# Kernel tuning notes

Hardware: AMD Instinct MI355X
Metric: run time of the kernel (lower is better)

The kernel has to match this reference:

```python
import jax, jax.numpy as jnp
import numpy as np

N = 120000
GRID = (480, 360, 32)
C_IN, C0, C1 = 16, 32, 64
EPS = 1e-5


def _build_rulebook(coords, lut, offsets, grid, n):
    # coords: [N,3] active voxel coords; lut: dense linear-index -> row (n = inactive)
    g = np.array(grid)
    cols = []
    for off in offsets:
        nc = coords + np.array(off)
        valid = np.all((nc >= 0) & (nc < g), axis=1)
        ncl = np.clip(nc, 0, g - 1)
        nlin = np.ravel_multi_index((ncl[:, 0], ncl[:, 1], ncl[:, 2]), grid)
        cols.append(np.where(valid, lut[nlin], n))
    return np.stack(cols, axis=1).astype(np.int32)  # [N, 9]


def setup_inputs() -> dict:
    rng = np.random.default_rng(0)
    total = GRID[0] * GRID[1] * GRID[2]
    lin = rng.choice(total, N, replace=False)
    coords = np.stack(np.unravel_index(lin, GRID), axis=1)
    lut = np.full(total, N, dtype=np.int32)
    lut[lin] = np.arange(N, dtype=np.int32)
    offs133 = [(0, dy, dz) for dy in (-1, 0, 1) for dz in (-1, 0, 1)]  # kernel (1,3,3)
    offs313 = [(dx, 0, dz) for dx in (-1, 0, 1) for dz in (-1, 0, 1)]  # kernel (3,1,3)
    nbr133 = jnp.asarray(_build_rulebook(coords, lut, offs133, GRID, N))
    nbr313 = jnp.asarray(_build_rulebook(coords, lut, offs313, GRID, N))

    key = jax.random.key(0)
    ks = jax.random.split(key, 9)

    def w(k, ci, co):
        return jax.random.normal(k, (9, ci, co), jnp.float32) * (1.0 / np.sqrt(9 * ci))

    ones = lambda c: jnp.ones((c,), jnp.float32)
    zeros = lambda c: jnp.zeros((c,), jnp.float32)
    return dict(
        x=jax.random.normal(ks[0], (N, C_IN), jnp.float32),
        nbr133=nbr133, nbr313=nbr313,
        W_c1=w(ks[1], C_IN, C0), g0=ones(C0), b0=zeros(C0),
        W_c12=w(ks[2], C0, C0), g02=ones(C0), b02=zeros(C0),
        W_c2=w(ks[3], C_IN, C0),
        W_c3=w(ks[4], C0, C0), g2=ones(C0), b2=zeros(C0),
        W_r1=w(ks[5], C0, C1), rg0=ones(C1), rb0=zeros(C1),
        W_r12=w(ks[6], C1, C1), rg02=ones(C1), rb02=zeros(C1),
        W_r2=w(ks[7], C0, C1), rg1=ones(C1), rb1=zeros(C1),
        W_r3=w(ks[8], C1, C1), rg2=ones(C1), rb2=zeros(C1),
    )


def _subm(x, nbr, W):
    # submanifold conv as rulebook gather-GEMM: pad row N with zeros for missing neighbors
    xp = jnp.concatenate([x, jnp.zeros((1, x.shape[1]), x.dtype)], axis=0)
    return jnp.einsum('nkc,kcd->nd', xp[nbr], W)  # [N, Cout]


def _bn(x, g, b):
    # BatchNorm1d over active voxels (training-mode batch stats, biased var)
    m = x.mean(axis=0)
    v = x.var(axis=0)
    return (x - m) / jnp.sqrt(v + EPS) * g + b


_lrelu = jax.nn.leaky_relu  # slope 0.01 = torch default


def reference(x, nbr133, nbr313, W_c1, g0, b0, W_c12, g02, b02, W_c2, W_c3, g2, b2,
              W_r1, rg0, rb0, W_r12, rg02, rb02, W_r2, rg1, rb1, W_r3, rg2, rb2):
    # ResContextBlock(16->32): conv -> act -> bn chains
    s = _bn(_lrelu(_subm(x, nbr133, W_c1)), g0, b0)
    s = _bn(_lrelu(_subm(s, nbr313, W_c12)), g02, b02)
    r = _lrelu(_subm(x, nbr313, W_c2))  # bn1 result discarded in source (reaA typo) -> faithfully skipped
    r = _bn(_lrelu(_subm(r, nbr133, W_c3)), g2, b2)
    y = r + s
    # ResBlock(32->64, pooling=False)
    s2 = _bn(_lrelu(_subm(y, nbr313, W_r1)), rg0, rb0)
    s2 = _bn(_lrelu(_subm(s2, nbr133, W_r12)), rg02, rb02)
    r2 = _bn(_lrelu(_subm(y, nbr133, W_r2)), rg1, rb1)
    r2 = _bn(_lrelu(_subm(r2, nbr313, W_r3)), rg2, rb2)
    return r2 + s2  # [N, 64]
```

## Files before the change

kernel.cpp:

```cpp
#include <hip/hip_runtime.h>
#include <hip/hip_bf16.h>

#define N_VOX 120000
#define NTILES (N_VOX / 16)

typedef __attribute__((ext_vector_type(8))) __bf16 bf16x8;
typedef __attribute__((ext_vector_type(4))) float floatx4;
using bf16 = __hip_bfloat16;

__device__ __forceinline__ float b2f(bf16 v) { return __bfloat162float(v); }
__device__ __forceinline__ bf16 f2b(float v) { return __float2bfloat16(v); }

__device__ __forceinline__ bf16x8 gload16(const bf16* p) {
    bf16x8 r;
    asm volatile("global_load_dwordx4 %0, %1, off" : "=v"(r) : "v"(p));
    return r;
}
__device__ __forceinline__ int gloadi(const int* p) {
    int r;
    asm volatile("global_load_dword %0, %1, off" : "=v"(r) : "v"(p));
    return r;
}
__device__ __forceinline__ void gstore16(bf16* p, bf16x8 v) {
    asm volatile("global_store_dwordx4 %0, %1, off" :: "v"(p), "v"(v) : "memory");
}
__device__ __forceinline__ void vm_wait0() { asm volatile("s_waitcnt vmcnt(0)" ::: "memory"); }
__device__ __forceinline__ void vm_wait1() { asm volatile("s_waitcnt vmcnt(1)" ::: "memory"); }
__device__ __forceinline__ void vm_wait2() { asm volatile("s_waitcnt vmcnt(2)" ::: "memory"); }
__device__ __forceinline__ void vm_wait3() { asm volatile("s_waitcnt vmcnt(3)" ::: "memory"); }
__device__ __forceinline__ void pin(bf16x8& x) { asm volatile("" : "+v"(x)); }
__device__ __forceinline__ void pini(int& x)   { asm volatile("" : "+v"(x)); }

template<int CIN, int COUT, int NW>
__device__ __forceinline__ void conv_body(
    const bf16* __restrict__ uin,
    const int*  __restrict__ nbr,
    const bf16* __restrict__ bpack,
    bf16* __restrict__ tout,
    float* __restrict__ stats, int bid, int nblk)
{
    constexpr int NT = COUT / 16;
    constexpr int K = 9 * CIN;
    constexpr int KSTEPS = (K + 31) / 32;
    constexpr bool BLDS = (COUT == 64);
    constexpr int NFRAG = KSTEPS * NT;
    constexpr int NSTORE = (16 * COUT) / 512;

    __shared__ bf16x8 Bs[BLDS ? NFRAG * 64 : 1];
    __shared__ int idxb[NW][2][192];
    __shared__ __align__(16) bf16 tbuf[NW][16 * COUT];
    __shared__ float sS[64], sS2[64];

    const int lane = threadIdx.x & 63;
    const int wave = threadIdx.x >> 6;
    const int m    = lane & 15;
    const int quad = lane >> 4;

    if (threadIdx.x < 64) { sS[threadIdx.x] = 0.f; sS2[threadIdx.x] = 0.f; }

    const bf16x8* bp = reinterpret_cast<const bf16x8*>(bpack);
    bf16x8 Bf[BLDS ? 1 : NFRAG];
    if constexpr (BLDS) {
        for (int f = threadIdx.x; f < NFRAG * 64; f += NW * 64) Bs[f] = bp[f];
    } else {
#pragma unroll
        for (int f = 0; f < NFRAG; ++f) Bf[f] = bp[f * 64 + lane];
    }
    __syncthreads();

    float ssum[NT], ssum2[NT];
#pragma unroll
    for (int c = 0; c < NT; ++c) { ssum[c] = 0.f; ssum2[c] = 0.f; }

    const int STRIDE = nblk * NW;
    const int t0 = bid * NW + wave;

    {
        const int* b0 = nbr + (size_t)t0 * 144;
        int i0 = gloadi(b0 + lane);
        int i1 = gloadi(b0 + 64 + lane);
        int i2 = gloadi(b0 + 128 + (lane & 15));
        vm_wait0();
        pini(i0); pini(i1); pini(i2);
        int* ib = idxb[wave][0];
        ib[lane] = i0; ib[64 + lane] = i1; ib[128 + (lane & 15)] = i2;
    }

    int p = 0;
    for (int tile = t0; tile < NTILES; tile += STRIDE) {
        const int* ib = idxb[wave][p];
        int idx[9];
#pragma unroll
        for (int nb = 0; nb < 9; ++nb) idx[nb] = ib[m * 9 + nb];

        bf16x8 a[KSTEPS];
#pragma unroll
        for (int t = 0; t < KSTEPS; ++t) {
            const bf16* src;
            if constexpr (CIN == 64) {
                src = uin + (((size_t)idx[t >> 1]) << 6) + ((t & 1) << 5) + quad * 8;
            } else if constexpr (CIN == 32) {
                src = uin + (((size_t)idx[t]) << 5) + quad * 8;
            } else {
                constexpr int KS = 9 * 16;
                const int j1 = (2 * t + 1 > 8) ? 8 : 2 * t + 1;
                int r_ = (quad & 2) ? idx[j1] : idx[2 * t];
                if (t * 32 + 24 >= KS) {
                    if (t * 32 + quad * 8 >= KS) r_ = N_VOX;
                }
                src = uin + (((size_t)r_) << 4) + ((quad & 1) << 3);
            }
            a[t] = gload16(src);
        }

        const int tnext = (tile + STRIDE < NTILES) ? tile + STRIDE : tile;
        const int* bn_ = nbr + (size_t)tnext * 144;
        int i0 = gloadi(bn_ + lane);
        int i1 = gloadi(bn_ + 64 + lane);
        int i2 = gloadi(bn_ + 128 + (lane & 15));

        vm_wait3();
#pragma unroll
        for (int t = 0; t < KSTEPS; ++t) pin(a[t]);

        floatx4 acc[NT];
#pragma unroll
        for (int c = 0; c < NT; ++c) acc[c] = (floatx4){0.f, 0.f, 0.f, 0.f};
#pragma unroll
        for (int t = 0; t < KSTEPS; ++t) {
#pragma unroll
            for (int c = 0; c < NT; ++c) {
                const bf16x8 b = BLDS ? Bs[(t * NT + c) * 64 + lane] : Bf[t * NT + c];
                acc[c] = __builtin_amdgcn_mfma_f32_16x16x32_bf16(a[t], b, acc[c], 0, 0, 0);
            }
        }

        bf16* tb = tbuf[wave];
#pragma unroll
        for (int c = 0; c < NT; ++c) {
            float ps = 0.f, ps2 = 0.f;
#pragma unroll
            for (int i = 0; i < 4; ++i) {
                float v = acc[c][i];
                v = v > 0.f ? v : 0.01f * v;
                tb[(quad * 4 + i) * COUT + c * 16 + m] = f2b(v);
                ps += v; ps2 += v * v;
            }
            ssum[c] += ps; ssum2[c] += ps2;
        }
#pragma unroll
        for (int g = 0; g < NSTORE; ++g) {
            const int off = g * 512 + lane * 8;
            bf16x8 row = *reinterpret_cast<const bf16x8*>(tb + off);
            gstore16(tout + (size_t)tile * (16 * COUT) + off, row);
        }

        if constexpr (NSTORE == 2) vm_wait2(); else vm_wait1();
        pini(i0); pini(i1); pini(i2);
        int* ibn = idxb[wave][p ^ 1];
        ibn[lane] = i0; ibn[64 + lane] = i1; ibn[128 + (lane & 15)] = i2;
        p ^= 1;
    }

    if (stats != nullptr) {
#pragma unroll
        for (int c = 0; c < NT; ++c) {
            atomicAdd(&sS[c * 16 + m], ssum[c]);
            atomicAdd(&sS2[c * 16 + m], ssum2[c]);
        }
        __syncthreads();
        if (threadIdx.x < COUT) {
            atomicAdd(&stats[threadIdx.x],      sS[threadIdx.x]);
            atomicAdd(&stats[64 + threadIdx.x], sS2[threadIdx.x]);
        }
    }
}

template<int CIN, int COUT, int NW>
__global__ __launch_bounds__(NW * 64) void conv_kernel(
    const bf16* __restrict__ uin, const int* __restrict__ nbr,
    const bf16* __restrict__ bpack, bf16* __restrict__ tout,
    float* __restrict__ stats)
{
    conv_body<CIN, COUT, NW>(uin, nbr, bpack, tout, stats, blockIdx.x, gridDim.x);
}

template<int CIN, int COUT, int NW>
__global__ __launch_bounds__(NW * 64) void conv2_kernel(
    int GA,
    const bf16* uinA, const int* nbrA, const bf16* bpA, bf16* toutA, float* stA,
    const bf16* uinB, const int* nbrB, const bf16* bpB, bf16* toutB, float* stB)
{
    const bool isB = (int)blockIdx.x >= GA;
    const int bid = isB ? (int)blockIdx.x - GA : (int)blockIdx.x;
    const bf16* uin   = isB ? uinB : uinA;
    const int*  nbr   = isB ? nbrB : nbrA;
    const bf16* bpack = isB ? bpB  : bpA;
    bf16*       tout  = isB ? toutB : toutA;
    float*      stats = isB ? stB  : stA;
    conv_body<CIN, COUT, NW>(uin, nbr, bpack, tout, stats, bid, GA);
}

template<int C>
__device__ __forceinline__ void bnapply_body(
    bf16* t, const float* __restrict__ s,
    const float* __restrict__ g, const float* __restrict__ b, int bid)
{
    __shared__ float pa[64], pc[64];
    if (threadIdx.x < C) {
        const float inv_n = 1.0f / N_VOX;
        const float mu = s[threadIdx.x] * inv_n;
        const float var = fmaxf(s[64 + threadIdx.x] * inv_n - mu * mu, 0.f);
        const float a = rsqrtf(var + 1e-5f) * g[threadIdx.x];
        pa[threadIdx.x] = a;
        pc[threadIdx.x] = b[threadIdx.x] - mu * a;
    }
    __syncthreads();
    const int i8 = (bid * 256 + threadIdx.x) * 8;
    if (i8 >= (N_VOX + 1) * C) return;
    if (i8 >= N_VOX * C) {
        uint4 z = {0, 0, 0, 0};
        *reinterpret_cast<uint4*>(t + i8) = z;
        return;
    }
    union { bf16x8 v; bf16 e[8]; } U, O;
    U.v = *reinterpret_cast<const bf16x8*>(t + i8);
    const int ch0 = i8 & (C - 1);
#pragma unroll
    for (int j = 0; j < 8; ++j)
        O.e[j] = f2b(pa[ch0 + j] * b2f(U.e[j]) + pc[ch0 + j]);
    *reinterpret_cast<bf16x8*>(t + i8) = O.v;
}

template<int C>
__global__ __launch_bounds__(256) void bnapply_kernel(
    bf16* t, const float* __restrict__ s,
    const float* __restrict__ g, const float* __restrict__ b)
{
    bnapply_body<C>(t, s, g, b, blockIdx.x);
}

__global__ __launch_bounds__(256) void bnapply2_kernel(
    int GA, bf16* tA, const float* sA, const float* gA, const float* bA,
    bf16* tB, const float* sB, const float* gB, const float* bB)
{
    const bool isB = (int)blockIdx.x >= GA;
    const int bid = isB ? (int)blockIdx.x - GA : (int)blockIdx.x;
    bnapply_body<64>(isB ? tB : tA, isB ? sB : sA, isB ? gB : gA,
                     isB ? bB : bA, bid);
}

template<int C, bool ZROW, typename OUT>
__global__ __launch_bounds__(256) void addbn_kernel(
    const bf16* ta, const float* __restrict__ sa,
    const float* __restrict__ ga, const float* __restrict__ ba,
    const bf16* tb, const float* __restrict__ sb,
    const float* __restrict__ gb, const float* __restrict__ bb,
    OUT* out)
{
    __shared__ float paa[64], pca[64], pab[64], pcb[64];
    if (threadIdx.x < C) {
        const float inv_n = 1.0f / N_VOX;
        const float ma = sa[threadIdx.x] * inv_n;
        const float va = fmaxf(sa[64 + threadIdx.x] * inv_n - ma * ma, 0.f);
        const float aa = rsqrtf(va + 1e-5f) * ga[threadIdx.x];
        paa[threadIdx.x] = aa;
        pca[threadIdx.x] = ba[threadIdx.x] - ma * aa;
        const float mb = sb[threadIdx.x] * inv_n;
        const float vb = fmaxf(sb[64 + threadIdx.x] * inv_n - mb * mb, 0.f);
        const float ab = rsqrtf(vb + 1e-5f) * gb[threadIdx.x];
        pab[threadIdx.x] = ab;
        pcb[threadIdx.x] = bb[threadIdx.x] - mb * ab;
    }
    __syncthreads();
    constexpr int TOTAL = (N_VOX + (ZROW ? 1 : 0)) * C;
    const int i8 = (blockIdx.x * 256 + threadIdx.x) * 8;
    if (i8 >= TOTAL) return;
    if (ZROW && i8 >= N_VOX * C) {
        uint4 z = {0, 0, 0, 0};
        *reinterpret_cast<uint4*>((bf16*)out + i8) = z;
        return;
    }
    union { bf16x8 v; bf16 e[8]; } A, B;
    A.v = *reinterpret_cast<const bf16x8*>(ta + i8);
    B.v = *reinterpret_cast<const bf16x8*>(tb + i8);
    const int ch0 = i8 & (C - 1);
    float r[8];
#pragma unroll
    for (int j = 0; j < 8; ++j)
        r[j] = paa[ch0 + j] * b2f(A.e[j]) + pca[ch0 + j]
             + pab[ch0 + j] * b2f(B.e[j]) + pcb[ch0 + j];
    if constexpr (sizeof(OUT) == 2) {
        union { bf16x8 v; bf16 e[8]; } O;
#pragma unroll
        for (int j = 0; j < 8; ++j) O.e[j] = f2b(r[j]);
        *reinterpret_cast<bf16x8*>(out + i8) = O.v;
    } else {
#pragma unroll
        for (int j = 0; j < 8; ++j) out[i8 + j] = r[j];
    }
}

#define PACK_TOTAL 139264
__global__ __launch_bounds__(256) void prep_kernel(
    const float* __restrict__ x,
    const float* W0, const float* W1, const float* W2, const float* W3,
    const float* W4, const float* W5, const float* W6, const float* W7,
    bf16* __restrict__ u0, bf16* __restrict__ bpack,
    float* __restrict__ stats, bf16* __restrict__ u3, bf16* __restrict__ u3b)
{
    const int gid = blockIdx.x * 256 + threadIdx.x;
    constexpr int NXE = (N_VOX + 1) * 16;
    if (gid < NXE) {
        u0[gid] = (gid < N_VOX * 16) ? f2b(x[gid]) : f2b(0.f);
        return;
    }
    int p = gid - NXE;
    if (p < PACK_TOTAL) {
        constexpr int cin[8]  = {16, 32, 16, 32, 32, 64, 32, 64};
        constexpr int cout[8] = {32, 32, 32, 32, 64, 64, 64, 64};
        constexpr int offs[9] = {0, 5120, 14336, 19456, 28672, 47104, 83968, 102400, 139264};
        const float* Ws[8] = {W0, W1, W2, W3, W4, W5, W6, W7};
        int w = 0;
        while (p >= offs[w + 1]) ++w;
        const int e = p - offs[w];
        const int CI = cin[w], CO = cout[w];
        const int NTl = CO / 16;
        const int j = e & 7;
        const int lane = (e >> 3) & 63;
        const int rest = e >> 9;
        const int c = rest % NTl;
        const int t = rest / NTl;
        const int ncol = c * 16 + (lane & 15);
        const int k = t * 32 + (lane >> 4) * 8 + j;
        float val = 0.f;
        if (k < 9 * CI) {
            const int nbq = k / CI;
            const int ci = k % CI;
            val = Ws[w][(nbq * CI + ci) * CO + ncol];
        }
        bpack[p] = f2b(val);
        return;
    }
    p -= PACK_TOTAL;
    if (p < 1024) { stats[p] = 0.f; return; }
    p -= 1024;
    if (p < 32) { u3[N_VOX * 32 + p] = f2b(0.f); return; }
    p -= 32;
    if (p < 32) u3b[N_VOX * 32 + p] = f2b(0.f);
}

extern "C" void kernel_launch(void* const* d_in, const int* in_sizes, int n_in,
                              void* d_out, int out_size, void* d_ws, size_t ws_size,
                              hipStream_t stream) {
    const float* x     = (const float*)d_in[0];
    const int* nbr133  = (const int*)d_in[1];
    const int* nbr313  = (const int*)d_in[2];
    const float* W_c1  = (const float*)d_in[3];
    const float* g0    = (const float*)d_in[4];
    const float* b0    = (const float*)d_in[5];
    const float* W_c12 = (const float*)d_in[6];
    const float* g02   = (const float*)d_in[7];
    const float* b02   = (const float*)d_in[8];
    const float* W_c2  = (const float*)d_in[9];
    const float* W_c3  = (const float*)d_in[10];
    const float* g2    = (const float*)d_in[11];
    const float* b2    = (const float*)d_in[12];
    const float* W_r1  = (const float*)d_in[13];
    const float* rg0   = (const float*)d_in[14];
    const float* rb0   = (const float*)d_in[15];
    const float* W_r12 = (const float*)d_in[16];
    const float* rg02  = (const float*)d_in[17];
    const float* rb02  = (const float*)d_in[18];
    const float* W_r2  = (const float*)d_in[19];
    const float* rg1   = (const float*)d_in[20];
    const float* rb1   = (const float*)d_in[21];
    const float* W_r3  = (const float*)d_in[22];
    const float* rg2   = (const float*)d_in[23];
    const float* rb2   = (const float*)d_in[24];

    char* ws = (char*)d_ws;
    size_t off = 0;
    auto alloc = [&](size_t bytes) -> char* {
        off = (off + 255) & ~(size_t)255;
        char* p = ws + off;
        off += bytes;
        return p;
    };
    const size_t NV = N_VOX;
    bf16* u0   = (bf16*)alloc((NV + 1) * 16 * 2);
    bf16* B1u3 = (bf16*)alloc((NV + 1) * 32 * 2);
    bf16* T4   = (bf16*)alloc(NV * 32 * 2);
    bf16* T2uy = (bf16*)alloc((NV + 1) * 32 * 2);
    bf16* B5B7 = (bf16*)alloc((NV + 1) * 64 * 2);
    bf16* T8   = (bf16*)alloc(NV * 64 * 2);
    bf16* bpack = (bf16*)alloc((size_t)PACK_TOTAL * 2);
    float* stats = (float*)alloc(1024 * 4);
    bf16* T9   = (bf16*)alloc(NV * 64 * 2);
    bf16* T6 = (bf16*)ws;

    float* st1 = stats + 0 * 128;
    float* st2 = stats + 1 * 128;
    float* st4 = stats + 3 * 128;
    float* st5 = stats + 4 * 128;
    float* st6 = stats + 5 * 128;
    float* st7 = stats + 6 * 128;
    float* st8 = stats + 7 * 128;

    bf16* bp0 = bpack + 0;
    bf16* bp1 = bpack + 5120;
    bf16* bp2 = bpack + 14336;
    bf16* bp3 = bpack + 19456;
    bf16* bp4 = bpack + 28672;
    bf16* bp5 = bpack + 47104;
    bf16* bp6 = bpack + 83968;
    bf16* bp7 = bpack + 102400;

    const int prep_total = (N_VOX + 1) * 16 + PACK_TOTAL + 1024 + 32 + 32;
    prep_kernel<<<(prep_total + 255) / 256, 256, 0, stream>>>(
        x, W_c1, W_c12, W_c2, W_c3, W_r1, W_r12, W_r2, W_r3,
        u0, bpack, stats, B1u3, T2uy);

    const int E32 = (((N_VOX + 1) * 32) / 8 + 255) / 256;
    const int E64 = (((N_VOX + 1) * 64) / 8 + 255) / 256;

    conv2_kernel<16, 32, 4><<<1536, 256, 0, stream>>>(
        768, u0, nbr133, bp0, B1u3, st1, u0, nbr313, bp2, T2uy, nullptr);
    bnapply_kernel<32><<<E32, 256, 0, stream>>>(B1u3, st1, g0, b0);
    conv2_kernel<32, 32, 4><<<1536, 256, 0, stream>>>(
        768, B1u3, nbr313, bp1, T4, st2, T2uy, nbr133, bp3, B5B7, st4);
    addbn_kernel<32, true, bf16><<<E32, 256, 0, stream>>>(
        T4, st2, g02, b02, B5B7, st4, g2, b2, T2uy);
    conv2_kernel<32, 64, 8><<<512, 512, 0, stream>>>(
        256, T2uy, nbr313, bp4, B5B7, st5, T2uy, nbr133, bp6, T8, st7);
    bnapply2_kernel<<<2 * E64, 256, 0, stream>>>(
        E64, B5B7, st5, rg0, rb0, T8, st7, rg1, rb1);
    conv2_kernel<64, 64, 16><<<256, 1024, 0, stream>>>(
        128, B5B7, nbr133, bp5, T6, st6, T8, nbr313, bp7, T9, st8);
    addbn_kernel<64, false, float><<<((N_VOX * 64 / 8) + 255) / 256, 256, 0, stream>>>(
        T6, st6, rg02, rb02, T9, st8, rg2, rb2, (float*)d_out);
}
```

Measured before the change: 261.3 us.

## Fold BatchNorm affine into next conv weights and per-neighbor bias

Removes the standalone BN-apply passes over the 32- and 64-channel activations. The BN scale is folded into repacked conv weights by small repack kernels, and the BN shift is applied as a per-neighbor bias added inside the conv only for valid neighbors. This saves full read-modify-write passes over large activation tensors. In exchange it adds small repack launches, bias-mask work in the conv epilogue, and extra LDS, and rounding now happens on the scaled weights rather than the normalized activations.

```diff
diff --git a/kernel.cpp b/kernel.cpp
--- a/kernel.cpp
+++ b/kernel.cpp
@@ -31,13 +31,15 @@
 __device__ __forceinline__ void pin(bf16x8& x) { asm volatile("" : "+v"(x)); }
 __device__ __forceinline__ void pini(int& x)   { asm volatile("" : "+v"(x)); }
 
-template<int CIN, int COUT, int NW>
+template<int CIN, int COUT, int NW, bool BIAS>
 __device__ __forceinline__ void conv_body(
     const bf16* __restrict__ uin,
     const int*  __restrict__ nbr,
     const bf16* __restrict__ bpack,
     bf16* __restrict__ tout,
-    float* __restrict__ stats, int bid, int nblk)
+    float* __restrict__ stats,
+    const float* __restrict__ biasT,
+    int bid, int nblk)
 {
     constexpr int NT = COUT / 16;
     constexpr int K = 9 * CIN;
@@ -50,6 +52,7 @@
     __shared__ int idxb[NW][2][192];
     __shared__ __align__(16) bf16 tbuf[NW][16 * COUT];
     __shared__ float sS[64], sS2[64];
+    __shared__ float biasL[BIAS ? 9 * COUT : 1];
 
     const int lane = threadIdx.x & 63;
     const int wave = threadIdx.x >> 6;
@@ -57,6 +60,12 @@
     const int quad = lane >> 4;
 
     if (threadIdx.x < 64) { sS[threadIdx.x] = 0.f; sS2[threadIdx.x] = 0.f; }
+
+    const bool useBias = BIAS && (biasT != nullptr);
+    if constexpr (BIAS) {
+        if (biasT != nullptr)
+            for (int f = threadIdx.x; f < 9 * COUT; f += NW * 64) biasL[f] = biasT[f];
+    }
 
     const bf16x8* bp = reinterpret_cast<const bf16x8*>(bpack);
     bf16x8 Bf[BLDS ? 1 : NFRAG];
@@ -135,6 +144,29 @@
             }
         }
 
+        if (useBias) {
+            unsigned vm_[4];
+#pragma unroll
+            for (int i = 0; i < 4; ++i) {
+                const int r = quad * 4 + i;
+                unsigned v = 0;
+#pragma unroll
+                for (int nb = 0; nb < 9; ++nb)
+                    v |= (ib[r * 9 + nb] != N_VOX) ? (1u << nb) : 0u;
+                vm_[i] = v;
+            }
+#pragma unroll
+            for (int c = 0; c < NT; ++c) {
+#pragma unroll
+                for (int nb = 0; nb < 9; ++nb) {
+                    const float bl = biasL[nb * COUT + c * 16 + m];
+#pragma unroll
+                    for (int i = 0; i < 4; ++i)
+                        acc[c][i] += ((vm_[i] >> nb) & 1u) ? bl : 0.f;
+                }
+            }
+        }
+
         bf16* tb = tbuf[wave];
 #pragma unroll
         for (int c = 0; c < NT; ++c) {
@@ -176,20 +208,13 @@
     }
 }
 
-template<int CIN, int COUT, int NW>
-__global__ __launch_bounds__(NW * 64) void conv_kernel(
-    const bf16* __restrict__ uin, const int* __restrict__ nbr,
-    const bf16* __restrict__ bpack, bf16* __restrict__ tout,
-    float* __restrict__ stats)
-{
-    conv_body<CIN, COUT, NW>(uin, nbr, bpack, tout, stats, blockIdx.x, gridDim.x);
-}
-
-template<int CIN, int COUT, int NW>
+template<int CIN, int COUT, int NW, bool BIAS>
 __global__ __launch_bounds__(NW * 64) void conv2_kernel(
     int GA,
-    const bf16* uinA, const int* nbrA, const bf16* bpA, bf16* toutA, float* stA,
-    const bf16* uinB, const int* nbrB, const bf16* bpB, bf16* toutB, float* stB)
+    const bf16* uinA, const int* nbrA, const bf16* bpA, bf16* toutA,
+    float* stA, const float* biA,
+    const bf16* uinB, const int* nbrB, const bf16* bpB, bf16* toutB,
+    float* stB, const float* biB)
 {
     const bool isB = (int)blockIdx.x >= GA;
     const int bid = isB ? (int)blockIdx.x - GA : (int)blockIdx.x;
@@ -198,56 +223,73 @@
     const bf16* bpack = isB ? bpB  : bpA;
     bf16*       tout  = isB ? toutB : toutA;
     float*      stats = isB ? stB  : stA;
-    conv_body<CIN, COUT, NW>(uin, nbr, bpack, tout, stats, bid, GA);
-}
-
-template<int C>
-__device__ __forceinline__ void bnapply_body(
-    bf16* t, const float* __restrict__ s,
-    const float* __restrict__ g, const float* __restrict__ b, int bid)
-{
-    __shared__ float pa[64], pc[64];
-    if (threadIdx.x < C) {
-        const float inv_n = 1.0f / N_VOX;
-        const float mu = s[threadIdx.x] * inv_n;
-        const float var = fmaxf(s[64 + threadIdx.x] * inv_n - mu * mu, 0.f);
-        const float a = rsqrtf(var + 1e-5f) * g[threadIdx.x];
-        pa[threadIdx.x] = a;
-        pc[threadIdx.x] = b[threadIdx.x] - mu * a;
-    }
-    __syncthreads();
-    const int i8 = (bid * 256 + threadIdx.x) * 8;
-    if (i8 >= (N_VOX + 1) * C) return;
-    if (i8 >= N_VOX * C) {
-        uint4 z = {0, 0, 0, 0};
-        *reinterpret_cast<uint4*>(t + i8) = z;
+    const float* bi   = isB ? biB : biA;
+    conv_body<CIN, COUT, NW, BIAS>(uin, nbr, bpack, tout, stats, bi, bid, GA);
+}
+
+template<int CI, int CO>
+__device__ __forceinline__ void repack_one(
+    const float* __restrict__ W, const float* __restrict__ s,
+    const float* __restrict__ g, const float* __restrict__ b,
+    bf16* __restrict__ outPack, float* __restrict__ outBias, int e)
+{
+    constexpr int NTl = CO / 16;
+    constexpr int KST = (9 * CI + 31) / 32;
+    constexpr int NPACK = KST * NTl * 512;
+    const float inv_n = 1.0f / N_VOX;
+    if (e < NPACK) {
+        const int j = e & 7;
+        const int lane = (e >> 3) & 63;
+        const int rest = e >> 9;
+        const int c = rest % NTl;
+        const int t = rest / NTl;
+        const int ncol = c * 16 + (lane & 15);
+        const int k = t * 32 + (lane >> 4) * 8 + j;
+        float val = 0.f;
+        if (k < 9 * CI) {
+            const int nbq = k / CI, ci = k % CI;
+            const float mu = s[ci] * inv_n;
+            const float var = fmaxf(s[64 + ci] * inv_n - mu * mu, 0.f);
+            const float pa = rsqrtf(var + 1e-5f) * g[ci];
+            val = pa * W[(nbq * CI + ci) * CO + ncol];
+        }
+        outPack[e] = f2b(val);
         return;
     }
-    union { bf16x8 v; bf16 e[8]; } U, O;
-    U.v = *reinterpret_cast<const bf16x8*>(t + i8);
-    const int ch0 = i8 & (C - 1);
-#pragma unroll
-    for (int j = 0; j < 8; ++j)
-        O.e[j] = f2b(pa[ch0 + j] * b2f(U.e[j]) + pc[ch0 + j]);
-    *reinterpret_cast<bf16x8*>(t + i8) = O.v;
-}
-
-template<int C>
-__global__ __launch_bounds__(256) void bnapply_kernel(
-    bf16* t, const float* __restrict__ s,
-    const float* __restrict__ g, const float* __restrict__ b)
-{
-    bnapply_body<C>(t, s, g, b, blockIdx.x);
-}
-
-__global__ __launch_bounds__(256) void bnapply2_kernel(
-    int GA, bf16* tA, const float* sA, const float* gA, const float* bA,
-    bf16* tB, const float* sB, const float* gB, const float* bB)
-{
-    const bool isB = (int)blockIdx.x >= GA;
-    const int bid = isB ? (int)blockIdx.x - GA : (int)blockIdx.x;
-    bnapply_body<64>(isB ? tB : tA, isB ? sB : sA, isB ? gB : gA,
-                     isB ? bB : bA, bid);
+    const int eb = e - NPACK;
+    const int nb = eb / CO, co = eb % CO;
+    float bs = 0.f;
+    for (int ci = 0; ci < CI; ++ci) {
+        const float mu = s[ci] * inv_n;
+        const float var = fmaxf(s[64 + ci] * inv_n - mu * mu, 0.f);
+        const float pa = rsqrtf(var + 1e-5f) * g[ci];
+        const float pc = b[ci] - mu * pa;
+        bs += pc * W[(nb * CI + ci) * CO + co];
+    }
+    outBias[eb] = bs;
+}
+
+template<int CI, int CO>
+__global__ __launch_bounds__(256) void repack_kernel(
+    const float* W, const float* s, const float* g, const float* b,
+    bf16* outPack, float* outBias)
+{
+    constexpr int TOT = ((9 * CI + 31) / 32) * (CO / 16) * 512 + 9 * CO;
+    const int e = blockIdx.x * 256 + threadIdx.x;
+    if (e < TOT) repack_one<CI, CO>(W, s, g, b, outPack, outBias, e);
+}
+
+template<int CI, int CO>
+__global__ __launch_bounds__(256) void repack2_kernel(
+    const float* WA, const float* sA, const float* gA, const float* bA,
+    bf16* packA, float* biasA,
+    const float* WB, const float* sB, const float* gB, const float* bB,
+    bf16* packB, float* biasB)
+{
+    constexpr int TOT = ((9 * CI + 31) / 32) * (CO / 16) * 512 + 9 * CO;
+    const int e = blockIdx.x * 256 + threadIdx.x;
+    if (e < TOT)            repack_one<CI, CO>(WA, sA, gA, bA, packA, biasA, e);
+    else if (e < 2 * TOT)   repack_one<CI, CO>(WB, sB, gB, bB, packB, biasB, e - TOT);
 }
 
 template<int C, bool ZROW, typename OUT>
@@ -307,7 +349,8 @@
     const float* W0, const float* W1, const float* W2, const float* W3,
     const float* W4, const float* W5, const float* W6, const float* W7,
     bf16* __restrict__ u0, bf16* __restrict__ bpack,
-    float* __restrict__ stats, bf16* __restrict__ u3, bf16* __restrict__ u3b)
+    float* __restrict__ stats, bf16* __restrict__ u3, bf16* __restrict__ u3b,
+    bf16* __restrict__ p64a, bf16* __restrict__ p64b)
 {
     const int gid = blockIdx.x * 256 + threadIdx.x;
     constexpr int NXE = (N_VOX + 1) * 16;
@@ -347,7 +390,11 @@
     p -= 1024;
     if (p < 32) { u3[N_VOX * 32 + p] = f2b(0.f); return; }
     p -= 32;
-    if (p < 32) u3b[N_VOX * 32 + p] = f2b(0.f);
+    if (p < 32) { u3b[N_VOX * 32 + p] = f2b(0.f); return; }
+    p -= 32;
+    if (p < 64) { p64a[(size_t)N_VOX * 64 + p] = f2b(0.f); return; }
+    p -= 64;
+    if (p < 64) p64b[(size_t)N_VOX * 64 + p] = f2b(0.f);
 }
 
 extern "C" void kernel_launch(void* const* d_in, const int* in_sizes, int n_in,
@@ -393,10 +440,16 @@
     bf16* T4   = (bf16*)alloc(NV * 32 * 2);
     bf16* T2uy = (bf16*)alloc((NV + 1) * 32 * 2);
     bf16* B5B7 = (bf16*)alloc((NV + 1) * 64 * 2);
-    bf16* T8   = (bf16*)alloc(NV * 64 * 2);
+    bf16* T8   = (bf16*)alloc((NV + 1) * 64 * 2);
     bf16* bpack = (bf16*)alloc((size_t)PACK_TOTAL * 2);
     float* stats = (float*)alloc(1024 * 4);
     bf16* T9   = (bf16*)alloc(NV * 64 * 2);
+    bf16* bp1s = (bf16*)alloc(9216 * 2);
+    float* bias1 = (float*)alloc(288 * 4);
+    bf16* bp5s = (bf16*)alloc(36864 * 2);
+    float* bias5 = (float*)alloc(576 * 4);
+    bf16* bp7s = (bf16*)alloc(36864 * 2);
+    float* bias7 = (float*)alloc(576 * 4);
     bf16* T6 = (bf16*)ws;
 
     float* st1 = stats + 0 * 128;
@@ -408,35 +461,36 @@
     float* st8 = stats + 7 * 128;
 
     bf16* bp0 = bpack + 0;
-    bf16* bp1 = bpack + 5120;
     bf16* bp2 = bpack + 14336;
     bf16* bp3 = bpack + 19456;
     bf16* bp4 = bpack + 28672;
-    bf16* bp5 = bpack + 47104;
     bf16* bp6 = bpack + 83968;
-    bf16* bp7 = bpack + 102400;
-
-    const int prep_total = (N_VOX + 1) * 16 + PACK_TOTAL + 1024 + 32 + 32;
+
+    const int prep_total = (N_VOX + 1) * 16 + PACK_TOTAL + 1024 + 32 + 32 + 64 + 64;
     prep_kernel<<<(prep_total + 255) / 256, 256, 0, stream>>>(
         x, W_c1, W_c12, W_c2, W_c3, W_r1, W_r12, W_r2, W_r3,
-        u0, bpack, stats, B1u3, T2uy);
+        u0, bpack, stats, B1u3, T2uy, B5B7, T8);
 
     const int E32 = (((N_VOX + 1) * 32) / 8 + 255) / 256;
-    const int E64 = (((N_VOX + 1) * 64) / 8 + 255) / 256;
-
-    conv2_kernel<16, 32, 4><<<1536, 256, 0, stream>>>(
-        768, u0, nbr133, bp0, B1u3, st1, u0, nbr313, bp2, T2uy, nullptr);
-    bnapply_kernel<32><<<E32, 256, 0, stream>>>(B1u3, st1, g0, b0);
-    conv2_kernel<32, 32, 4><<<1536, 256, 0, stream>>>(
-        768, B1u3, nbr313, bp1, T4, st2, T2uy, nbr133, bp3, B5B7, st4);
+
+    conv2_kernel<16, 32, 4, false><<<1536, 256, 0, stream>>>(
+        768, u0, nbr133, bp0, B1u3, st1, nullptr,
+             u0, nbr313, bp2, T2uy, nullptr, nullptr);
+    repack_kernel<32, 32><<<38, 256, 0, stream>>>(W_c12, st1, g0, b0, bp1s, bias1);
+    conv2_kernel<32, 32, 4, true><<<1536, 256, 0, stream>>>(
+        768, B1u3, nbr313, bp1s, T4, st2, bias1,
+             T2uy, nbr133, bp3, B5B7, st4, nullptr);
     addbn_kernel<32, true, bf16><<<E32, 256, 0, stream>>>(
         T4, st2, g02, b02, B5B7, st4, g2, b2, T2uy);
-    conv2_kernel<32, 64, 8><<<512, 512, 0, stream>>>(
-        256, T2uy, nbr313, bp4, B5B7, st5, T2uy, nbr133, bp6, T8, st7);
-    bnapply2_kernel<<<2 * E64, 256, 0, stream>>>(
-        E64, B5B7, st5, rg0, rb0, T8, st7, rg1, rb1);
-    conv2_kernel<64, 64, 16><<<256, 1024, 0, stream>>>(
-        128, B5B7, nbr133, bp5, T6, st6, T8, nbr313, bp7, T9, st8);
+    conv2_kernel<32, 64, 8, false><<<512, 512, 0, stream>>>(
+        256, T2uy, nbr313, bp4, B5B7, st5, nullptr,
+             T2uy, nbr133, bp6, T8, st7, nullptr);
+    repack2_kernel<64, 64><<<293, 256, 0, stream>>>(
+        W_r12, st5, rg0, rb0, bp5s, bias5,
+        W_r3,  st7, rg1, rb1, bp7s, bias7);
+    conv2_kernel<64, 64, 16, true><<<256, 1024, 0, stream>>>(
+        128, B5B7, nbr133, bp5s, T6, st6, bias5,
+             T8, nbr313, bp7s, T9, st8, bias7);
     addbn_kernel<64, false, float><<<((N_VOX * 64 / 8) + 255) / 256, 256, 0, stream>>>(
         T6, st6, rg02, rb02, T9, st8, rg2, rb2, (float*)d_out);
 }
```

After: 267.6 us. +2.4%, slower.
